# Performance work log

Hardware: AMD Instinct MI355X
Metric: run time of the kernel (lower is better)

The kernel has to match this reference:

```python
import jax, jax.numpy as jnp
import numpy as np

B, I, HID, H, KS = 64, 1024, 2048, 8, 4
D = HID // H  # head_size = 256; also BlockDiagonal block size = (2*I)//H = 256
EPS = 1e-5


def setup_inputs() -> dict:
    key = jax.random.key(0)
    ks = jax.random.split(key, 16)
    r = lambda i, shape, s=0.02: jax.random.normal(ks[i], shape, dtype=jnp.float32) * s
    z = lambda shape: jnp.zeros(shape, jnp.float32)
    return {
        "x": jax.random.normal(ks[0], (B, I), dtype=jnp.float32),
        "h_prev": z((B, H, D)),
        "c_prev": z((B, H, D, D)),
        "n_prev": z((B, H, D)),
        "m_prev": z((B, H)),
        "ln_w": jnp.ones((I,), jnp.float32), "ln_b": z((I,)),
        "W_ul": r(1, (I, HID)), "b_ul": z((HID,)),
        "W_ur": r(2, (I, HID)), "b_ur": z((HID,)),
        "W_conv": r(3, (HID, HID, KS)), "b_conv": z((HID,)),
        "W_skip": r(4, (HID, HID)), "b_skip": z((HID,)),
        "W_q": r(5, (H, D, D)), "b_q": z((HID,)),
        "W_k": r(6, (H, D, D)), "b_k": z((HID,)),
        "W_v": r(7, (H, D, D)), "b_v": z((HID,)),
        "W_i": r(8, (HID, H)), "b_i": z((H,)),
        "W_f": r(9, (HID, H)), "b_f": z((H,)),
        "W_o": r(10, (HID, HID)), "b_o": z((HID,)),
        "W_down": r(11, (HID, I)), "b_down": z((I,)),
        "gn_w": jnp.ones((HID,), jnp.float32), "gn_b": z((HID,)),
    }


def _block_diag(zf, W, b):
    # BlockDiagonal: chunk last dim into H blocks, per-block Linear, concat -> [B,H,D]
    zh = zf.reshape(zf.shape[0], H, -1)
    return jnp.einsum('bhi,hio->bho', zh, W) + b.reshape(H, -1)


def reference(x, h_prev, c_prev, n_prev, m_prev, ln_w, ln_b, W_ul, b_ul, W_ur, b_ur,
              W_conv, b_conv, W_skip, b_skip, W_q, b_q, W_k, b_k, W_v, b_v,
              W_i, b_i, W_f, b_f, W_o, b_o, W_down, b_down, gn_w, gn_b):
    # LayerNorm
    mu = x.mean(-1, keepdims=True)
    var = jnp.mean((x - mu) ** 2, -1, keepdims=True)
    xn = (x - mu) * jax.lax.rsqrt(var + EPS) * ln_w + ln_b
    # Up projections
    xl = xn @ W_ul + b_ul            # [B, 2I] == [B, HID]
    xr = xn @ W_ur + b_ur
    # Causal conv over a length-1 sequence: after left padding + slicing, only the
    # last kernel tap (index KS-1) touches real data -> linear map with W_conv[:,:,KS-1]
    xc = jax.nn.silu(xl @ W_conv[:, :, KS - 1].T + b_conv)
    x_skip = xc @ W_skip + b_skip    # [B, HID]
    q = _block_diag(xc, W_q, b_q)                       # [B,H,D]
    k = _block_diag(xc, W_k, b_k) / jnp.sqrt(jnp.float32(D))
    v = _block_diag(xl, W_v, b_v)
    i_t = xc @ W_i + b_i             # [B,H]
    f_t = xc @ W_f + b_f
    o = jax.nn.sigmoid(xl @ W_o + b_o).reshape(-1, H, D)
    # Stabilized exponential gating
    m_t = jnp.maximum(f_t + m_prev, i_t)
    i_g = jnp.exp(i_t - m_t)
    f_g = jnp.exp(f_t + m_prev - m_t)
    # Outer-product state update + bilinear readout
    c_t = f_g[..., None, None] * c_prev + i_g[..., None, None] * jnp.einsum('bhd,bhk->bhdk', v, k)
    n_t = f_g[..., None] * n_prev + i_g[..., None] * k
    num = jnp.einsum('bhdk,bhk->bhd', c_t, q)
    den = jnp.clip(jnp.einsum('bhd,bhd->bh', n_t, q), 1.0, None)[..., None]
    h_t = o * num / den              # [B,H,D]
    # GroupNorm with num_groups == num_heads: normalize per head
    g_mu = h_t.mean(-1, keepdims=True)
    g_var = jnp.mean((h_t - g_mu) ** 2, -1, keepdims=True)
    gn = ((h_t - g_mu) * jax.lax.rsqrt(g_var + EPS)).reshape(-1, HID) * gn_w + gn_b
    out = (gn + x_skip) * jax.nn.silu(xr)
    out = out @ W_down + b_down
    final = out + x
    return (final, h_t, c_t, n_t, m_t)
```

## Files before the change

### kernel.cpp

```cpp
#include <hip/hip_runtime.h>
#include <cstddef>

typedef __bf16 bf16;
typedef __bf16 bf16x8 __attribute__((ext_vector_type(8)));
typedef short  s16x8  __attribute__((ext_vector_type(8)));
typedef float  f32x4  __attribute__((ext_vector_type(4)));

template <class T> T&& declv() noexcept;
template <class, class = void> struct takes_bf16vec { static constexpr bool value = false; };
template <class V> struct takes_bf16vec<V, decltype((void)__builtin_amdgcn_mfma_f32_16x16x32_bf16(
    declv<V>(), declv<V>(), declv<f32x4>(), 0, 0, 0))> { static constexpr bool value = true; };

template <class V>
__device__ __forceinline__ f32x4 mfma_bf16_16x16x32(V a, V b, f32x4 c) {
  if constexpr (takes_bf16vec<V>::value) {
    return __builtin_amdgcn_mfma_f32_16x16x32_bf16(a, b, c, 0, 0, 0);
  } else {
    return __builtin_amdgcn_mfma_f32_16x16x32_bf16(
        __builtin_bit_cast(s16x8, a), __builtin_bit_cast(s16x8, b), c, 0, 0, 0);
  }
}

constexpr int M_NONE = 0, M_SILU = 1, M_SIG = 2;

__global__ __launch_bounds__(256) void ln_kernel(const float* __restrict__ x,
                                                 const float* __restrict__ w,
                                                 const float* __restrict__ bs,
                                                 const float* __restrict__ bdown,
                                                 bf16* __restrict__ xn,
                                                 float* __restrict__ outf) {
  const int b = blockIdx.x, tid = threadIdx.x;
  __shared__ float red[256];
  float vals[4];
  float s = 0.f;
#pragma unroll
  for (int i = 0; i < 4; ++i) { vals[i] = x[b * 1024 + i * 256 + tid]; s += vals[i]; }
  red[tid] = s; __syncthreads();
  for (int off = 128; off; off >>= 1) { if (tid < off) red[tid] += red[tid + off]; __syncthreads(); }
  const float mu = red[0] * (1.f / 1024.f);
  __syncthreads();
  float s2 = 0.f;
#pragma unroll
  for (int i = 0; i < 4; ++i) { const float d = vals[i] - mu; s2 += d * d; }
  red[tid] = s2; __syncthreads();
  for (int off = 128; off; off >>= 1) { if (tid < off) red[tid] += red[tid + off]; __syncthreads(); }
  const float rs = rsqrtf(red[0] * (1.f / 1024.f) + 1e-5f);
#pragma unroll
  for (int i = 0; i < 4; ++i) {
    const int j = i * 256 + tid;
    xn[b * 1024 + j] = (bf16)((vals[i] - mu) * rs * w[j] + bs[j]);
    outf[b * 1024 + j] = vals[i] + bdown[j];
  }
}

template <int K, bool TAP>
__device__ __forceinline__ void gemm_tile(
    const bf16* __restrict__ A, int ldA, int aOff,
    const float* __restrict__ W, int ldB, int wcol,
    const float* __restrict__ bias, int bOff, float scale, int mode,
    float* __restrict__ outF, bf16* __restrict__ outB, int outLd, int oOff,
    float lds[4][64][20]) {
  const int tid = threadIdx.x;
  const int lane = tid & 63, wave = tid >> 6;
  const int l15 = lane & 15, quad = lane >> 4;
  constexpr int chunk = K / 4;
  const int kbeg = wave * chunk;
  f32x4 acc0{}, acc1{}, acc2{}, acc3{};
#pragma unroll 4
  for (int k = 0; k < chunk; k += 32) {
    const int kk = kbeg + k + quad * 8;
    bf16x8 bfrag;
    if (TAP) {
      const float* wp = W + ((size_t)(wcol + l15) * K + kk) * 4 + 3;
#pragma unroll
      for (int j = 0; j < 8; ++j) bfrag[j] = (bf16)wp[j * 4];
    } else {
      const float* wp = W + (size_t)kk * ldB + wcol + l15;
#pragma unroll
      for (int j = 0; j < 8; ++j) bfrag[j] = (bf16)wp[(size_t)j * ldB];
    }
    const bf16* ap = A + (size_t)l15 * ldA + aOff + kk;
    const size_t st = (size_t)16 * ldA;
    bf16x8 a0 = *(const bf16x8*)(ap);
    bf16x8 a1 = *(const bf16x8*)(ap + st);
    bf16x8 a2 = *(const bf16x8*)(ap + 2 * st);
    bf16x8 a3 = *(const bf16x8*)(ap + 3 * st);
    acc0 = mfma_bf16_16x16x32(a0, bfrag, acc0);
    acc1 = mfma_bf16_16x16x32(a1, bfrag, acc1);
    acc2 = mfma_bf16_16x16x32(a2, bfrag, acc2);
    acc3 = mfma_bf16_16x16x32(a3, bfrag, acc3);
  }
#pragma unroll
  for (int r = 0; r < 4; ++r) {
    const int rr = quad * 4 + r;
    lds[wave][rr][l15]      = acc0[r];
    lds[wave][16 + rr][l15] = acc1[r];
    lds[wave][32 + rr][l15] = acc2[r];
    lds[wave][48 + rr][l15] = acc3[r];
  }
  __syncthreads();
  const int col = tid & 15, rb = (tid >> 4) << 2;
  const float bvv = bias[bOff + col];
#pragma unroll
  for (int r2 = 0; r2 < 4; ++r2) {
    const int row = rb + r2;
    float v = (lds[0][row][col] + lds[1][row][col] + lds[2][row][col] + lds[3][row][col] + bvv) * scale;
    if (mode == M_SILU)      v = v / (1.f + expf(-v));
    else if (mode == M_SIG)  v = 1.f / (1.f + expf(-v));
    const size_t oi = (size_t)row * outLd + oOff + col;
    if (outF) outF[oi] = v;
    if (outB) outB[oi] = (bf16)v;
  }
}

template <int K, bool TAP, bool DUAL>
__global__ __launch_bounds__(256) void gemm_full(
    const bf16* __restrict__ A0, const bf16* __restrict__ A1,
    const float* __restrict__ W0, const float* __restrict__ W1,
    int ldA, int ldB,
    const float* __restrict__ bias0, const float* __restrict__ bias1,
    int mode0, int mode1,
    float* __restrict__ outF0, bf16* __restrict__ outB0,
    float* __restrict__ outF1, bf16* __restrict__ outB1, int outLd) {
  __shared__ float lds[4][64][20];
  const int tile = blockIdx.x;
  if (DUAL) {
    const int ncol = (tile & 127) * 16;
    if (tile >> 7) {
      gemm_tile<K, TAP>(A1, ldA, 0, W1, ldB, ncol, bias1, ncol, 1.f, mode1,
                        outF1, outB1, outLd, ncol, lds);
    } else {
      gemm_tile<K, TAP>(A0, ldA, 0, W0, ldB, ncol, bias0, ncol, 1.f, mode0,
                        outF0, outB0, outLd, ncol, lds);
    }
  } else {
    const int ncol = tile * 16;
    gemm_tile<K, TAP>(A0, ldA, 0, W0, ldB, ncol, bias0, ncol, 1.f, mode0,
                      outF0, outB0, outLd, ncol, lds);
  }
}

__global__ __launch_bounds__(256) void mega_c(
    const bf16* __restrict__ xc, const bf16* __restrict__ xl,
    const float* __restrict__ W_skip, const float* __restrict__ b_skip,
    const float* __restrict__ W_o, const float* __restrict__ b_o,
    const float* __restrict__ Wq, const float* __restrict__ bq,
    const float* __restrict__ Wk, const float* __restrict__ bk,
    const float* __restrict__ Wv, const float* __restrict__ bv,
    const float* __restrict__ Wi, const float* __restrict__ bi,
    const float* __restrict__ Wf, const float* __restrict__ bfv,
    const float* __restrict__ m_prev,
    float* __restrict__ xskip_f, float* __restrict__ o_f,
    float* __restrict__ qf, float* __restrict__ kf, float* __restrict__ vf,
    float* __restrict__ ig, float* __restrict__ fgo, float* __restrict__ mt_out) {
  __shared__ float lds[4][64][20];
  const int bid = blockIdx.x;
  if (bid < 256) {
    const int seg = bid >> 7, ncol = (bid & 127) * 16;
    if (seg) {
      gemm_tile<2048, false>(xl, 2048, 0, W_o, 2048, ncol, b_o, ncol, 1.f, M_SIG,
                             o_f, nullptr, 2048, ncol, lds);
    } else {
      gemm_tile<2048, false>(xc, 2048, 0, W_skip, 2048, ncol, b_skip, ncol, 1.f, M_NONE,
                             xskip_f, nullptr, 2048, ncol, lds);
    }
  } else if (bid < 640) {
    const int t6 = bid - 256;
    const int seg = t6 >> 7, t = t6 & 127;
    const int n0 = t * 16, h = t >> 4;
    const bf16* A = (seg == 2) ? xl : xc;
    const float* W = (seg == 0) ? Wq : (seg == 1) ? Wk : Wv;
    const float* bias = (seg == 0) ? bq : (seg == 1) ? bk : bv;
    float* out = (seg == 0) ? qf : (seg == 1) ? kf : vf;
    gemm_tile<256, false>(A, 2048, h << 8, W + (size_t)h * 65536, 256, n0 & 255,
                          bias, n0, (seg == 1) ? 0.0625f : 1.f, M_NONE,
                          out, nullptr, 2048, n0, lds);
  } else {
    const int b = bid - 640, tid = threadIdx.x;
    float* shf = &lds[0][0][0];
    float (*ri)[8] = reinterpret_cast<float(*)[8]>(shf);
    float (*rf)[8] = reinterpret_cast<float(*)[8]>(shf + 2048);
    float ai[8] = {}, af[8] = {};
    for (int k = tid; k < 2048; k += 256) {
      const float xv = (float)xc[b * 2048 + k];
      const float4 wi0 = *(const float4*)(Wi + (size_t)k * 8);
      const float4 wi1 = *(const float4*)(Wi + (size_t)k * 8 + 4);
      const float4 wf0 = *(const float4*)(Wf + (size_t)k * 8);
      const float4 wf1 = *(const float4*)(Wf + (size_t)k * 8 + 4);
      ai[0] += xv * wi0.x; ai[1] += xv * wi0.y; ai[2] += xv * wi0.z; ai[3] += xv * wi0.w;
      ai[4] += xv * wi1.x; ai[5] += xv * wi1.y; ai[6] += xv * wi1.z; ai[7] += xv * wi1.w;
      af[0] += xv * wf0.x; af[1] += xv * wf0.y; af[2] += xv * wf0.z; af[3] += xv * wf0.w;
      af[4] += xv * wf1.x; af[5] += xv * wf1.y; af[6] += xv * wf1.z; af[7] += xv * wf1.w;
    }
#pragma unroll
    for (int h = 0; h < 8; ++h) { ri[tid][h] = ai[h]; rf[tid][h] = af[h]; }
    __syncthreads();
    for (int off = 128; off; off >>= 1) {
      if (tid < off) {
#pragma unroll
        for (int h = 0; h < 8; ++h) { ri[tid][h] += ri[tid + off][h]; rf[tid][h] += rf[tid + off][h]; }
      }
      __syncthreads();
    }
    if (tid < 8) {
      const float it = ri[0][tid] + bi[tid];
      const float ft = rf[0][tid] + bfv[tid];
      const float mp = m_prev[b * 8 + tid];
      const float mt = fmaxf(ft + mp, it);
      mt_out[b * 8 + tid] = mt;
      ig[b * 8 + tid] = expf(it - mt);
      fgo[b * 8 + tid] = expf(ft + mp - mt);
    }
  }
}

__global__ __launch_bounds__(256) void state_fused(
    const float* __restrict__ c_prev, const float* __restrict__ n_prev,
    const float* __restrict__ qf, const float* __restrict__ kf,
    const float* __restrict__ vf, const float* __restrict__ of,
    const float* __restrict__ ig, const float* __restrict__ fg,
    const float* __restrict__ xskip, const float* __restrict__ xrf,
    const float* __restrict__ gnw, const float* __restrict__ gnb,
    float* __restrict__ ct_out, float* __restrict__ nt_out,
    float* __restrict__ ht_out, bf16* __restrict__ pre_bf) {
  const int bh = blockIdx.x, b = bh >> 3, h = bh & 7;
  const int tid = threadIdx.x;
  const int vb = b * 2048 + h * 256;
  __shared__ float q_s[256], k_s[256], num_s[256], red[256];
  q_s[tid] = qf[vb + tid];
  k_s[tid] = kf[vb + tid];
  const float i_g = ig[bh], f_g = fg[bh];
  __syncthreads();
  const int lane8 = tid & 7, rowbase = tid >> 3;
#pragma unroll
  for (int rg = 0; rg < 8; ++rg) {
    const int row = rg * 32 + rowbase;
    const float iv = i_g * vf[vb + row];
    const size_t base = ((size_t)bh << 16) + ((size_t)row << 8) + lane8 * 4;
    float p = 0.f;
#pragma unroll
    for (int i = 0; i < 8; ++i) {
      const int c = lane8 * 4 + i * 32;
      const float4 cp = *(const float4*)(c_prev + base + i * 32);
      float4 cn;
      cn.x = f_g * cp.x + iv * k_s[c];
      cn.y = f_g * cp.y + iv * k_s[c + 1];
      cn.z = f_g * cp.z + iv * k_s[c + 2];
      cn.w = f_g * cp.w + iv * k_s[c + 3];
      *(float4*)(ct_out + base + i * 32) = cn;
      p += cn.x * q_s[c] + cn.y * q_s[c + 1] + cn.z * q_s[c + 2] + cn.w * q_s[c + 3];
    }
    p += __shfl_xor(p, 1, 64);
    p += __shfl_xor(p, 2, 64);
    p += __shfl_xor(p, 4, 64);
    if (lane8 == 0) num_s[row] = p;
  }
  __syncthreads();
  const float qv = q_s[tid], kv = k_s[tid];
  const float nv = f_g * n_prev[bh * 256 + tid] + i_g * kv;
  nt_out[bh * 256 + tid] = nv;
  red[tid] = nv * qv;
  __syncthreads();
  for (int off = 128; off; off >>= 1) { if (tid < off) red[tid] += red[tid + off]; __syncthreads(); }
  const float den = fmaxf(red[0], 1.0f);
  const float hv = of[vb + tid] * num_s[tid] / den;
  ht_out[bh * 256 + tid] = hv;
  __syncthreads();
  red[tid] = hv; __syncthreads();
  for (int off = 128; off; off >>= 1) { if (tid < off) red[tid] += red[tid + off]; __syncthreads(); }
  const float mu = red[0] * (1.f / 256.f);
  __syncthreads();
  const float dv = hv - mu;
  red[tid] = dv * dv; __syncthreads();
  for (int off = 128; off; off >>= 1) { if (tid < off) red[tid] += red[tid + off]; __syncthreads(); }
  const float gn = (hv - mu) * rsqrtf(red[0] * (1.f / 256.f) + 1e-5f);
  const int j = h * 256 + tid;
  const float xr = xrf[b * 2048 + j];
  const float pre = (gn * gnw[j] + gnb[j] + xskip[b * 2048 + j]) * (xr / (1.f + expf(-xr)));
  pre_bf[b * 2048 + j] = (bf16)pre;
}

template <int K, int KS, int NTILES>
__global__ __launch_bounds__(256) void gemm_atomic(
    const bf16* __restrict__ A, const float* __restrict__ W,
    int ldA, int ldB, float* __restrict__ dst, int outN) {
  constexpr int Kslice = K / KS;
  constexpr int chunk = Kslice / 4;
  const int tid = threadIdx.x;
  const int lane = tid & 63, wave = tid >> 6;
  const int l15 = lane & 15, quad = lane >> 4;
  const int tile = blockIdx.x % NTILES, ks = blockIdx.x / NTILES;
  const int ncol = tile * 16;
  const int kbeg = ks * Kslice + wave * chunk;

  f32x4 acc0{}, acc1{}, acc2{}, acc3{};
#pragma unroll
  for (int k = 0; k < chunk; k += 32) {
    const int kk = kbeg + k + quad * 8;
    bf16x8 bfrag;
    const float* wp = W + (size_t)kk * ldB + ncol + l15;
#pragma unroll
    for (int j = 0; j < 8; ++j) bfrag[j] = (bf16)wp[(size_t)j * ldB];
    const bf16* ap = A + (size_t)l15 * ldA + kk;
    const size_t st = (size_t)16 * ldA;
    bf16x8 a0 = *(const bf16x8*)(ap);
    bf16x8 a1 = *(const bf16x8*)(ap + st);
    bf16x8 a2 = *(const bf16x8*)(ap + 2 * st);
    bf16x8 a3 = *(const bf16x8*)(ap + 3 * st);
    acc0 = mfma_bf16_16x16x32(a0, bfrag, acc0);
    acc1 = mfma_bf16_16x16x32(a1, bfrag, acc1);
    acc2 = mfma_bf16_16x16x32(a2, bfrag, acc2);
    acc3 = mfma_bf16_16x16x32(a3, bfrag, acc3);
  }
  __shared__ float lds[4][64][20];
#pragma unroll
  for (int r = 0; r < 4; ++r) {
    const int rr = quad * 4 + r;
    lds[wave][rr][l15]      = acc0[r];
    lds[wave][16 + rr][l15] = acc1[r];
    lds[wave][32 + rr][l15] = acc2[r];
    lds[wave][48 + rr][l15] = acc3[r];
  }
  __syncthreads();
  const int col = tid & 15, rb = (tid >> 4) << 2;
#pragma unroll
  for (int r2 = 0; r2 < 4; ++r2) {
    const int row = rb + r2;
    const float v = lds[0][row][col] + lds[1][row][col] + lds[2][row][col] + lds[3][row][col];
    atomicAdd(dst + (size_t)row * outN + ncol + col, v);
  }
}

extern "C" void kernel_launch(void* const* d_in, const int* in_sizes, int n_in,
                              void* d_out, int out_size, void* d_ws, size_t ws_size,
                              hipStream_t stream) {
  (void)in_sizes; (void)n_in; (void)out_size; (void)ws_size;
  const float* x      = (const float*)d_in[0];
  const float* c_prev = (const float*)d_in[2];
  const float* n_prev = (const float*)d_in[3];
  const float* m_prev = (const float*)d_in[4];
  const float* ln_w = (const float*)d_in[5];
  const float* ln_b = (const float*)d_in[6];
  const float* W_ul = (const float*)d_in[7];
  const float* b_ul = (const float*)d_in[8];
  const float* W_ur = (const float*)d_in[9];
  const float* b_ur = (const float*)d_in[10];
  const float* W_conv = (const float*)d_in[11];
  const float* b_conv = (const float*)d_in[12];
  const float* W_skip = (const float*)d_in[13];
  const float* b_skip = (const float*)d_in[14];
  const float* W_q = (const float*)d_in[15];
  const float* b_q = (const float*)d_in[16];
  const float* W_k = (const float*)d_in[17];
  const float* b_k = (const float*)d_in[18];
  const float* W_v = (const float*)d_in[19];
  const float* b_v = (const float*)d_in[20];
  const float* W_i = (const float*)d_in[21];
  const float* b_i = (const float*)d_in[22];
  const float* W_f = (const float*)d_in[23];
  const float* b_f = (const float*)d_in[24];
  const float* W_o = (const float*)d_in[25];
  const float* b_o = (const float*)d_in[26];
  const float* W_down = (const float*)d_in[27];
  const float* b_down = (const float*)d_in[28];
  const float* gn_w = (const float*)d_in[29];
  const float* gn_b = (const float*)d_in[30];

  float* out_final = (float*)d_out;
  float* out_ht = out_final + 65536;
  float* out_ct = out_final + 196608;
  float* out_nt = out_final + 33751040;
  float* out_mt = out_final + 33882112;

  char* ws = (char*)d_ws;
  bf16*  xn_bf   = (bf16*)(ws + 0);
  bf16*  xl_bf   = (bf16*)(ws + 131072);
  bf16*  xc_bf   = (bf16*)(ws + 393216);
  bf16*  pre_bf  = (bf16*)(ws + 655360);
  float* xr_f    = (float*)(ws + 917504);
  float* xskip_f = (float*)(ws + 1441792);
  float* q_f     = (float*)(ws + 1966080);
  float* k_f     = (float*)(ws + 2490368);
  float* v_f     = (float*)(ws + 3014656);
  float* o_f     = (float*)(ws + 3538944);
  float* ig_f    = (float*)(ws + 4063232);
  float* fg_f    = (float*)(ws + 4065280);

  ln_kernel<<<64, 256, 0, stream>>>(x, ln_w, ln_b, b_down, xn_bf, out_final);
  gemm_full<1024, false, true><<<256, 256, 0, stream>>>(
      xn_bf, xn_bf, W_ul, W_ur, 1024, 2048,
      b_ul, b_ur, M_NONE, M_NONE, nullptr, xl_bf, xr_f, nullptr, 2048);
  gemm_full<2048, true, false><<<128, 256, 0, stream>>>(
      xl_bf, nullptr, W_conv, nullptr, 2048, 0,
      b_conv, nullptr, M_SILU, M_NONE, nullptr, xc_bf, nullptr, nullptr, 2048);
  mega_c<<<704, 256, 0, stream>>>(
      xc_bf, xl_bf, W_skip, b_skip, W_o, b_o, W_q, b_q, W_k, b_k, W_v, b_v,
      W_i, b_i, W_f, b_f, m_prev, xskip_f, o_f, q_f, k_f, v_f, ig_f, fg_f, out_mt);
  state_fused<<<512, 256, 0, stream>>>(
      c_prev, n_prev, q_f, k_f, v_f, o_f, ig_f, fg_f,
      xskip_f, xr_f, gn_w, gn_b, out_ct, out_nt, out_ht, pre_bf);
  gemm_atomic<2048, 8, 64><<<512, 256, 0, stream>>>(
      pre_bf, W_down, 2048, 1024, out_final, 1024);
}
```

Measured before the change: 424.9 us.

## Widen up-proj and conv GEMMs to 8 waves, narrow conv tiles, swizzle block order

The up-projection GEMM now runs 512-thread blocks, so eight waves split K instead of four. The conv GEMM gets its own kernel that computes 8 output columns per block across 256 blocks, where before it used 128 blocks, so more CUs work on the strided fp32 weight reads. The block index is also remapped with an XCD-aware swizzle (blockIdx&7 stride) in the up-projection, mega_c and atomic down-projection kernels, to keep related tiles on the same chiplet's L2. The costs are extra LDS reduction work and a conv MFMA in which half the B columns are duplicates.

```diff
diff --git a/kernel.cpp b/kernel.cpp
--- a/kernel.cpp
+++ b/kernel.cpp
@@ -53,32 +53,26 @@
   }
 }
 
-template <int K, bool TAP>
+template <int K, int NW>
 __device__ __forceinline__ void gemm_tile(
     const bf16* __restrict__ A, int ldA, int aOff,
     const float* __restrict__ W, int ldB, int wcol,
     const float* __restrict__ bias, int bOff, float scale, int mode,
     float* __restrict__ outF, bf16* __restrict__ outB, int outLd, int oOff,
-    float lds[4][64][20]) {
+    float lds[NW][64][20]) {
   const int tid = threadIdx.x;
   const int lane = tid & 63, wave = tid >> 6;
   const int l15 = lane & 15, quad = lane >> 4;
-  constexpr int chunk = K / 4;
+  constexpr int chunk = K / NW;
   const int kbeg = wave * chunk;
   f32x4 acc0{}, acc1{}, acc2{}, acc3{};
 #pragma unroll 4
   for (int k = 0; k < chunk; k += 32) {
     const int kk = kbeg + k + quad * 8;
     bf16x8 bfrag;
-    if (TAP) {
-      const float* wp = W + ((size_t)(wcol + l15) * K + kk) * 4 + 3;
-#pragma unroll
-      for (int j = 0; j < 8; ++j) bfrag[j] = (bf16)wp[j * 4];
-    } else {
-      const float* wp = W + (size_t)kk * ldB + wcol + l15;
-#pragma unroll
-      for (int j = 0; j < 8; ++j) bfrag[j] = (bf16)wp[(size_t)j * ldB];
-    }
+    const float* wp = W + (size_t)kk * ldB + wcol + l15;
+#pragma unroll
+    for (int j = 0; j < 8; ++j) bfrag[j] = (bf16)wp[(size_t)j * ldB];
     const bf16* ap = A + (size_t)l15 * ldA + aOff + kk;
     const size_t st = (size_t)16 * ldA;
     bf16x8 a0 = *(const bf16x8*)(ap);
@@ -99,44 +93,91 @@
     lds[wave][48 + rr][l15] = acc3[r];
   }
   __syncthreads();
-  const int col = tid & 15, rb = (tid >> 4) << 2;
-  const float bvv = bias[bOff + col];
-#pragma unroll
-  for (int r2 = 0; r2 < 4; ++r2) {
-    const int row = rb + r2;
-    float v = (lds[0][row][col] + lds[1][row][col] + lds[2][row][col] + lds[3][row][col] + bvv) * scale;
-    if (mode == M_SILU)      v = v / (1.f + expf(-v));
-    else if (mode == M_SIG)  v = 1.f / (1.f + expf(-v));
-    const size_t oi = (size_t)row * outLd + oOff + col;
-    if (outF) outF[oi] = v;
-    if (outB) outB[oi] = (bf16)v;
-  }
-}
-
-template <int K, bool TAP, bool DUAL>
-__global__ __launch_bounds__(256) void gemm_full(
-    const bf16* __restrict__ A0, const bf16* __restrict__ A1,
-    const float* __restrict__ W0, const float* __restrict__ W1,
-    int ldA, int ldB,
-    const float* __restrict__ bias0, const float* __restrict__ bias1,
-    int mode0, int mode1,
-    float* __restrict__ outF0, bf16* __restrict__ outB0,
-    float* __restrict__ outF1, bf16* __restrict__ outB1, int outLd) {
-  __shared__ float lds[4][64][20];
-  const int tile = blockIdx.x;
-  if (DUAL) {
-    const int ncol = (tile & 127) * 16;
-    if (tile >> 7) {
-      gemm_tile<K, TAP>(A1, ldA, 0, W1, ldB, ncol, bias1, ncol, 1.f, mode1,
-                        outF1, outB1, outLd, ncol, lds);
-    } else {
-      gemm_tile<K, TAP>(A0, ldA, 0, W0, ldB, ncol, bias0, ncol, 1.f, mode0,
-                        outF0, outB0, outLd, ncol, lds);
-    }
+  if (tid < 256) {
+    const int col = tid & 15, rb = (tid >> 4) << 2;
+    const float bvv = bias[bOff + col];
+#pragma unroll
+    for (int r2 = 0; r2 < 4; ++r2) {
+      const int row = rb + r2;
+      float v = bvv;
+#pragma unroll
+      for (int w = 0; w < NW; ++w) v += lds[w][row][col];
+      v *= scale;
+      if (mode == M_SILU)      v = v / (1.f + expf(-v));
+      else if (mode == M_SIG)  v = 1.f / (1.f + expf(-v));
+      const size_t oi = (size_t)row * outLd + oOff + col;
+      if (outF) outF[oi] = v;
+      if (outB) outB[oi] = (bf16)v;
+    }
+  }
+}
+
+__global__ __launch_bounds__(512) void gemm_ulur(
+    const bf16* __restrict__ xn,
+    const float* __restrict__ W_ul, const float* __restrict__ W_ur,
+    const float* __restrict__ b_ul, const float* __restrict__ b_ur,
+    bf16* __restrict__ xl_bf, float* __restrict__ xr_f) {
+  __shared__ float lds[8][64][20];
+  const int l = (blockIdx.x & 7) * 32 + (blockIdx.x >> 3);
+  const int ncol = (l & 127) * 16;
+  if (l >> 7) {
+    gemm_tile<1024, 8>(xn, 1024, 0, W_ur, 2048, ncol, b_ur, ncol, 1.f, M_NONE,
+                       xr_f, nullptr, 2048, ncol, lds);
   } else {
-    const int ncol = tile * 16;
-    gemm_tile<K, TAP>(A0, ldA, 0, W0, ldB, ncol, bias0, ncol, 1.f, mode0,
-                      outF0, outB0, outLd, ncol, lds);
+    gemm_tile<1024, 8>(xn, 1024, 0, W_ul, 2048, ncol, b_ul, ncol, 1.f, M_NONE,
+                       nullptr, xl_bf, 2048, ncol, lds);
+  }
+}
+
+__global__ __launch_bounds__(512) void gemm_conv(
+    const bf16* __restrict__ xl, const float* __restrict__ Wc,
+    const float* __restrict__ bc, bf16* __restrict__ xc) {
+  __shared__ float lds[8][64][20];
+  const int tid = threadIdx.x;
+  const int lane = tid & 63, wave = tid >> 6;
+  const int l15 = lane & 15, quad = lane >> 4;
+  const int n0 = blockIdx.x * 8;
+  const int kbeg = wave * 256;
+  f32x4 acc0{}, acc1{}, acc2{}, acc3{};
+#pragma unroll 4
+  for (int k = 0; k < 256; k += 32) {
+    const int kk = kbeg + k + quad * 8;
+    bf16x8 bfrag;
+    const float* wp = Wc + ((size_t)(n0 + (l15 & 7)) * 2048 + kk) * 4 + 3;
+#pragma unroll
+    for (int j = 0; j < 8; ++j) bfrag[j] = (bf16)wp[j * 4];
+    const bf16* ap = xl + (size_t)l15 * 2048 + kk;
+    const size_t st = (size_t)16 * 2048;
+    bf16x8 a0 = *(const bf16x8*)(ap);
+    bf16x8 a1 = *(const bf16x8*)(ap + st);
+    bf16x8 a2 = *(const bf16x8*)(ap + 2 * st);
+    bf16x8 a3 = *(const bf16x8*)(ap + 3 * st);
+    acc0 = mfma_bf16_16x16x32(a0, bfrag, acc0);
+    acc1 = mfma_bf16_16x16x32(a1, bfrag, acc1);
+    acc2 = mfma_bf16_16x16x32(a2, bfrag, acc2);
+    acc3 = mfma_bf16_16x16x32(a3, bfrag, acc3);
+  }
+#pragma unroll
+  for (int r = 0; r < 4; ++r) {
+    const int rr = quad * 4 + r;
+    lds[wave][rr][l15]      = acc0[r];
+    lds[wave][16 + rr][l15] = acc1[r];
+    lds[wave][32 + rr][l15] = acc2[r];
+    lds[wave][48 + rr][l15] = acc3[r];
+  }
+  __syncthreads();
+  if (tid < 128) {
+    const int col = tid & 7, rb = (tid >> 3) << 2;
+    const float bvv = bc[n0 + col];
+#pragma unroll
+    for (int r2 = 0; r2 < 4; ++r2) {
+      const int row = rb + r2;
+      float v = bvv;
+#pragma unroll
+      for (int w = 0; w < 8; ++w) v += lds[w][row][col];
+      v = v / (1.f + expf(-v));
+      xc[(size_t)row * 2048 + n0 + col] = (bf16)v;
+    }
   }
 }
 
@@ -154,15 +195,15 @@
     float* __restrict__ qf, float* __restrict__ kf, float* __restrict__ vf,
     float* __restrict__ ig, float* __restrict__ fgo, float* __restrict__ mt_out) {
   __shared__ float lds[4][64][20];
-  const int bid = blockIdx.x;
+  const int bid = (blockIdx.x & 7) * 88 + (blockIdx.x >> 3);
   if (bid < 256) {
     const int seg = bid >> 7, ncol = (bid & 127) * 16;
     if (seg) {
-      gemm_tile<2048, false>(xl, 2048, 0, W_o, 2048, ncol, b_o, ncol, 1.f, M_SIG,
-                             o_f, nullptr, 2048, ncol, lds);
+      gemm_tile<2048, 4>(xl, 2048, 0, W_o, 2048, ncol, b_o, ncol, 1.f, M_SIG,
+                         o_f, nullptr, 2048, ncol, lds);
     } else {
-      gemm_tile<2048, false>(xc, 2048, 0, W_skip, 2048, ncol, b_skip, ncol, 1.f, M_NONE,
-                             xskip_f, nullptr, 2048, ncol, lds);
+      gemm_tile<2048, 4>(xc, 2048, 0, W_skip, 2048, ncol, b_skip, ncol, 1.f, M_NONE,
+                         xskip_f, nullptr, 2048, ncol, lds);
     }
   } else if (bid < 640) {
     const int t6 = bid - 256;
@@ -172,9 +213,9 @@
     const float* W = (seg == 0) ? Wq : (seg == 1) ? Wk : Wv;
     const float* bias = (seg == 0) ? bq : (seg == 1) ? bk : bv;
     float* out = (seg == 0) ? qf : (seg == 1) ? kf : vf;
-    gemm_tile<256, false>(A, 2048, h << 8, W + (size_t)h * 65536, 256, n0 & 255,
-                          bias, n0, (seg == 1) ? 0.0625f : 1.f, M_NONE,
-                          out, nullptr, 2048, n0, lds);
+    gemm_tile<256, 4>(A, 2048, h << 8, W + (size_t)h * 65536, 256, n0 & 255,
+                      bias, n0, (seg == 1) ? 0.0625f : 1.f, M_NONE,
+                      out, nullptr, 2048, n0, lds);
   } else {
     const int b = bid - 640, tid = threadIdx.x;
     float* shf = &lds[0][0][0];
@@ -289,7 +330,8 @@
   const int tid = threadIdx.x;
   const int lane = tid & 63, wave = tid >> 6;
   const int l15 = lane & 15, quad = lane >> 4;
-  const int tile = blockIdx.x % NTILES, ks = blockIdx.x / NTILES;
+  const int l = (blockIdx.x & 7) * ((NTILES * KS) / 8) + (blockIdx.x >> 3);
+  const int tile = l % NTILES, ks = l / NTILES;
   const int ncol = tile * 16;
   const int kbeg = ks * Kslice + wave * chunk;
 
@@ -387,12 +429,8 @@
   float* fg_f    = (float*)(ws + 4065280);
 
   ln_kernel<<<64, 256, 0, stream>>>(x, ln_w, ln_b, b_down, xn_bf, out_final);
-  gemm_full<1024, false, true><<<256, 256, 0, stream>>>(
-      xn_bf, xn_bf, W_ul, W_ur, 1024, 2048,
-      b_ul, b_ur, M_NONE, M_NONE, nullptr, xl_bf, xr_f, nullptr, 2048);
-  gemm_full<2048, true, false><<<128, 256, 0, stream>>>(
-      xl_bf, nullptr, W_conv, nullptr, 2048, 0,
-      b_conv, nullptr, M_SILU, M_NONE, nullptr, xc_bf, nullptr, nullptr, 2048);
+  gemm_ulur<<<256, 512, 0, stream>>>(xn_bf, W_ul, W_ur, b_ul, b_ur, xl_bf, xr_f);
+  gemm_conv<<<256, 512, 0, stream>>>(xl_bf, W_conv, b_conv, xc_bf);
   mega_c<<<704, 256, 0, stream>>>(
       xc_bf, xl_bf, W_skip, b_skip, W_o, b_o, W_q, b_q, W_k, b_k, W_v, b_v,
       W_i, b_i, W_f, b_f, m_prev, xskip_f, o_f, q_f, k_f, v_f, ig_f, fg_f, out_mt);
```

After: 442.2 us. +4.1%, slower.
